# Kernel tuning notes

Measured on AMD Instinct MI355X. Metric: run time of the kernel, lower is better.

The kernel has to match this reference:

```python
import jax, jax.numpy as jnp
import numpy as np

B, N, T, NIN = 2048, 8, 20, 2
ES, HS, NL, NEMB = 64, 128, 3, 64


def setup_inputs() -> dict:
    key = jax.random.key(0)
    ks = jax.random.split(key, 12)
    def nrm(k, shape, scale=1.0):
        return jax.random.normal(k, shape, dtype=jnp.float32) * scale
    s_in = 1.0 / np.sqrt(HS)
    return {
        "x": nrm(ks[0], (B, N, T, NIN)),
        "pos_enc_agents": nrm(ks[1], (N,)),
        "pos_enc_time": nrm(ks[2], (T,)),
        "emb_W": nrm(ks[3], (ES, NIN), 1.0 / np.sqrt(NIN)),
        "emb_b": nrm(ks[4], (ES,), 0.01),
        "Wih0": nrm(ks[5], (3 * HS, ES), s_in),
        "Wih_rest": nrm(ks[6], (NL - 1, 3 * HS, HS), s_in),
        "Whh": nrm(ks[7], (NL, 3 * HS, HS), s_in),
        "bih": nrm(ks[8], (NL, 3 * HS), s_in),
        "bhh": nrm(ks[9], (NL, 3 * HS), s_in),
        "out_W": nrm(ks[10], (NEMB, HS), s_in),
        "out_b": nrm(ks[11], (NEMB,), 0.01),
    }


def _gru_layer(xs, Wih, Whh, bih, bhh):
    # xs: [M, T, in]; PyTorch GRU gate order (r, z, n)
    gi = jnp.einsum('mti,gi->mtg', xs, Wih) + bih  # precompute input gates [M,T,3H]
    H = Whh.shape[-1]

    def step(h, g):
        gh = h @ Whh.T + bhh
        ir, iz, inn = jnp.split(g, 3, axis=-1)
        hr, hz, hn = jnp.split(gh, 3, axis=-1)
        r = jax.nn.sigmoid(ir + hr)
        z = jax.nn.sigmoid(iz + hz)
        n = jnp.tanh(inn + r * hn)
        h_new = (1.0 - z) * n + z * h
        return h_new, h_new

    h0 = jnp.zeros((xs.shape[0], H), xs.dtype)
    hT, ys = jax.lax.scan(step, h0, jnp.swapaxes(gi, 0, 1))
    return jnp.swapaxes(ys, 0, 1), hT  # [M,T,H], [M,H]


def reference(x, pos_enc_agents, pos_enc_time, emb_W, emb_b,
              Wih0, Wih_rest, Whh, bih, bhh, out_W, out_b):
    b, n, t, _ = x.shape
    # positional encoding broadcast over batch and coord dims (p=2)
    pe = pos_enc_time[None, None, :, None] + pos_enc_agents[None, :, None, None]
    xe = jax.nn.relu(jnp.einsum('bntp,ep->bnte', x + pe, emb_W) + emb_b)
    # fold agents into batch: each agent starts from zero hidden state
    h = xe.reshape(b * n, t, -1)
    finals = []
    ys, hT = _gru_layer(h, Wih0, Whh[0], bih[0], bhh[0])
    finals.append(hT)
    for l in range(Wih_rest.shape[0]):
        ys, hT = _gru_layer(ys, Wih_rest[l], Whh[l + 1], bih[l + 1], bhh[l + 1])
        finals.append(hT)
    alpha = ys[:, -1]  # last timestep of top layer, [B*N, H]
    out = alpha @ out_W.T + out_b  # [B*N, nemb]
    # concat over agents along last dim, keep seq_len=1 dim like torch
    out = out.reshape(b, n * out_W.shape[0])[:, None, :]
    # hidden returned by torch is the final hidden of the LAST agent loop
    hidden = jnp.stack(finals).reshape(len(finals), b, n, -1)[:, :, -1]
    return out, hidden
```

## Files before the change

kernel.cpp:

```cpp
#include <hip/hip_runtime.h>
#include <hip/hip_bf16.h>


typedef _Float16 half8 __attribute__((ext_vector_type(8)));
typedef _Float16 half4 __attribute__((ext_vector_type(4)));
typedef float floatx4 __attribute__((ext_vector_type(4)));

#define MFMA16(a, b, c) __builtin_amdgcn_mfma_f32_16x16x32_f16((a), (b), (c), 0, 0, 0)

static __device__ __forceinline__ float ldin(const void* p, long i, bool f32) {
    return f32 ? ((const float*)p)[i]
               : __bfloat162float(((const __hip_bfloat16*)p)[i]);
}

static __device__ __forceinline__ bool detect_f32(const void* peT, const void* x) {
    const __hip_bfloat16* a = (const __hip_bfloat16*)peT;
    const __hip_bfloat16* b = (const __hip_bfloat16*)x;
    bool weird = false;
    for (int i = 0; i < 20; i++) {
        float v = fabsf(__bfloat162float(a[i]));
        if (!(v == 0.0f || (v > 1e-8f && v < 1e8f))) weird = true;
    }
    for (int i = 0; i < 64; i++) {
        float v = fabsf(__bfloat162float(b[i]));
        if (!(v == 0.0f || (v > 1e-8f && v < 1e8f))) weird = true;
    }
    return weird;
}

static __device__ __forceinline__ float fsigm(float x) {
    x = fminf(fmaxf(x, -60.f), 60.f);
    float e = __builtin_amdgcn_exp2f(-1.442695041f * x);
    return __builtin_amdgcn_rcpf(1.0f + e);
}
static __device__ __forceinline__ float ftanh(float x) {
    x = fminf(fmaxf(x, -30.f), 30.f);
    float e = __builtin_amdgcn_exp2f(2.885390082f * x);
    return 1.0f - 2.0f * __builtin_amdgcn_rcpf(1.0f + e);
}

__global__ __launch_bounds__(64) void prepack_kernel(
    const void* __restrict__ Whh,
    const void* __restrict__ WihR,
    const void* __restrict__ Wih0,
    const void* __restrict__ outW,
    const void* __restrict__ peT,
    const void* __restrict__ x,
    _Float16* __restrict__ ws)
{
    const bool f32 = detect_f32(peT, x);
    int fid  = blockIdx.x;
    int lane = threadIdx.x;
    int nlo = lane & 15, quad = lane >> 4;
    const void* src;
    long base;
    int row, k0, ldk;
    if (fid < 288) {
        int l = fid / 96, r = fid % 96;
        int ks = r & 3, q1 = r >> 2, g = q1 % 3, ctile = q1 / 3;
        row = g * 128 + ctile * 16 + nlo; k0 = ks * 32 + quad * 8; ldk = 128;
        src = Whh; base = (long)l * 384 * 128;
    } else if (fid < 480) {
        int f = fid - 288; int l = f / 96, r = f % 96;
        int ks = r & 3, q1 = r >> 2, g = q1 % 3, ctile = q1 / 3;
        row = g * 128 + ctile * 16 + nlo; k0 = ks * 32 + quad * 8; ldk = 128;
        src = WihR; base = (long)l * 384 * 128;
    } else if (fid < 528) {
        int r = fid - 480;
        int ks = r & 1, q1 = r >> 1, g = q1 % 3, ctile = q1 / 3;
        row = g * 128 + ctile * 16 + nlo; k0 = ks * 32 + quad * 8; ldk = 64;
        src = Wih0; base = 0;
    } else {
        int r = fid - 528; int ks = r & 3, ot = r >> 2;
        row = ot * 16 + nlo; k0 = ks * 32 + quad * 8; ldk = 128;
        src = outW; base = 0;
    }
    _Float16* d = ws + (long)fid * 512 + lane * 8;
#pragma unroll
    for (int j = 0; j < 8; j++)
        d[j] = (_Float16)ldin(src, base + (long)row * ldk + k0 + j, f32);
}

__global__ __launch_bounds__(768, 3) void rnn_fused(
    const void* __restrict__ x,
    const void* __restrict__ peA,
    const void* __restrict__ peT,
    const void* __restrict__ embW,
    const void* __restrict__ embB,
    const void* __restrict__ bih,
    const void* __restrict__ bhh,
    const void* __restrict__ outB,
    const _Float16* __restrict__ ws,
    float* __restrict__ out)
{
    __shared__ __align__(16) _Float16 hA[3][2][64][136];
    __shared__ __align__(16) _Float16 eA[2][64][72];
    __shared__ float emb0[64], emb1[64], embb[64];
    __shared__ float biasS[1536];

    const bool f32 = detect_f32(peT, x);

    const int tid  = threadIdx.x;
    const int w    = tid >> 6;
    const int lane = tid & 63;
    const int nlo  = lane & 15;
    const int quad = lane >> 4;
    const int qk   = quad * 8;
    const int m0   = blockIdx.x * 64;
    const int rot  = blockIdx.x & 3;
    const int ctr  = (blockIdx.x >> 2) & 1;

    for (int i = tid; i < 3 * 2 * 64 * 136; i += 768)
        (&hA[0][0][0][0])[i] = (_Float16)0.f;
    if (tid < 64) {
        emb0[tid] = ldin(embW, tid * 2 + 0, f32);
        emb1[tid] = ldin(embW, tid * 2 + 1, f32);
        embb[tid] = ldin(embB, tid, f32);
    }
    for (int idx = tid; idx < 1536; idx += 768) {
        int l = idx >> 9, r = idx & 511, g = r >> 7, c = r & 127;
        float v;
        if      (g == 0) v = ldin(bih, l * 384 + c, f32)       + ldin(bhh, l * 384 + c, f32);
        else if (g == 1) v = ldin(bih, l * 384 + 128 + c, f32) + ldin(bhh, l * 384 + 128 + c, f32);
        else if (g == 2) v = ldin(bih, l * 384 + 256 + c, f32);
        else             v = ldin(bhh, l * 384 + 256 + c, f32);
        biasS[idx] = v;
    }

    const int em = tid >> 2;
    const int ej = (tid & 3) * 16;
    const float peAg = ldin(peA, ((m0 + em) & 7), f32);

    __syncthreads();

#pragma unroll 1
    for (int s = 0; s < 23; s++) {
        const int l = w >> 2;
        const int W = w & 3;
        const int t = s - 1 - l;
        if (t >= 0 && t < 20) {
            const int p = (t + 1) & 1;
            const int q = t & 1;
            const int KGI = (l == 0) ? 2 : 4;
            const _Float16* inBase = (l == 0) ? &eA[t & 1][0][0]
                                              : &hA[l - 1][t & 1][0][0];
            const int inStride = (l == 0) ? 72 : 136;

#pragma unroll
            for (int ct0 = 0; ct0 < 2; ct0++) {
                const int c8 = W * 2 + ((ct0 + ctr) & 1);
                const int c4 = c8 * 16 + quad * 4;

                floatx4 acc[4][4];
#pragma unroll
                for (int g = 0; g < 4; g++) {
                    floatx4 b = *(const floatx4*)&biasS[(l * 4 + g) * 128 + c4];
#pragma unroll
                    for (int rt = 0; rt < 4; rt++) acc[g][rt] = b;
                }
#pragma unroll
                for (int ks0 = 0; ks0 < 4; ks0++) {
                    const int ks = (ks0 + rot) & 3;
                    half8 B0 = *(const half8*)&hA[l][p][0 * 16 + nlo][ks * 32 + qk];
                    half8 B1 = *(const half8*)&hA[l][p][1 * 16 + nlo][ks * 32 + qk];
                    half8 B2 = *(const half8*)&hA[l][p][2 * 16 + nlo][ks * 32 + qk];
                    half8 B3 = *(const half8*)&hA[l][p][3 * 16 + nlo][ks * 32 + qk];
#pragma unroll
                    for (int g = 0; g < 3; g++) {
                        const int ai = (g == 2) ? 3 : g;
                        half8 Wf = *(const half8*)(ws +
                            ((long)(l * 96 + (c8 * 3 + g) * 4 + ks)) * 512 + lane * 8);
                        acc[ai][0] = MFMA16(Wf, B0, acc[ai][0]);
                        acc[ai][1] = MFMA16(Wf, B1, acc[ai][1]);
                        acc[ai][2] = MFMA16(Wf, B2, acc[ai][2]);
                        acc[ai][3] = MFMA16(Wf, B3, acc[ai][3]);
                    }
                }
                for (int ks0 = 0; ks0 < KGI; ks0++) {
                    const int ks = (ks0 + rot) & (KGI - 1);
                    half8 B0 = *(const half8*)(inBase + (0 * 16 + nlo) * inStride + ks * 32 + qk);
                    half8 B1 = *(const half8*)(inBase + (1 * 16 + nlo) * inStride + ks * 32 + qk);
                    half8 B2 = *(const half8*)(inBase + (2 * 16 + nlo) * inStride + ks * 32 + qk);
                    half8 B3 = *(const half8*)(inBase + (3 * 16 + nlo) * inStride + ks * 32 + qk);
#pragma unroll
                    for (int g = 0; g < 3; g++) {
                        long f = (l == 0) ? (long)(480 + (c8 * 3 + g) * 2 + ks)
                                          : (long)(288 + (l - 1) * 96 + (c8 * 3 + g) * 4 + ks);
                        half8 Uf = *(const half8*)(ws + f * 512 + lane * 8);
                        acc[g][0] = MFMA16(Uf, B0, acc[g][0]);
                        acc[g][1] = MFMA16(Uf, B1, acc[g][1]);
                        acc[g][2] = MFMA16(Uf, B2, acc[g][2]);
                        acc[g][3] = MFMA16(Uf, B3, acc[g][3]);
                    }
                }
#pragma unroll
                for (int rt = 0; rt < 4; rt++) {
                    half4 ho = *(const half4*)&hA[l][p][rt * 16 + nlo][c4];
                    half4 hn;
#pragma unroll
                    for (int rg = 0; rg < 4; rg++) {
                        float r = fsigm(acc[0][rt][rg]);
                        float z = fsigm(acc[1][rt][rg]);
                        float n = ftanh(acc[2][rt][rg] + r * acc[3][rt][rg]);
                        hn[rg] = (_Float16)(n + z * ((float)ho[rg] - n));
                    }
                    *(half4*)&hA[l][q][rt * 16 + nlo][c4] = hn;
                }
            }
        }
        if (l == 0 && s < 20) {
            float x0 = ldin(x, ((long)(m0 + em) * 20 + s) * 2 + 0, f32);
            float x1 = ldin(x, ((long)(m0 + em) * 20 + s) * 2 + 1, f32);
            float pe = ldin(peT, s, f32) + peAg;
            float xp0 = x0 + pe, xp1 = x1 + pe;
#pragma unroll
            for (int jj = 0; jj < 16; jj++) {
                float e = fmaf(emb0[ej + jj], xp0, fmaf(emb1[ej + jj], xp1, embb[ej + jj]));
                eA[s & 1][em][ej + jj] = (_Float16)fmaxf(e, 0.f);
            }
        }
        __syncthreads();
    }

    if (w < 8) {
        const int otile = w & 3;
        const int rtb   = (w >> 2) * 2;
        half8 Ao[4];
#pragma unroll
        for (int ks = 0; ks < 4; ks++)
            Ao[ks] = *(const half8*)(ws + ((long)(528 + otile * 4 + ks)) * 512 + lane * 8);
        floatx4 ob;
#pragma unroll
        for (int rg = 0; rg < 4; rg++) ob[rg] = ldin(outB, otile * 16 + quad * 4 + rg, f32);
#pragma unroll
        for (int rr = 0; rr < 2; rr++) {
            const int rt = rtb + rr;
            floatx4 acc = ob;
#pragma unroll
            for (int ks = 0; ks < 4; ks++) {
                half8 b = *(const half8*)&hA[2][1][rt * 16 + nlo][ks * 32 + qk];
                acc = MFMA16(Ao[ks], b, acc);
            }
            *(floatx4*)&out[(long)(m0 + rt * 16 + nlo) * 64 + otile * 16 + quad * 4] = acc;
        }
    }

    for (int idx = tid; idx < 3 * 8 * 128; idx += 768) {
        int l2 = idx >> 10, r = idx & 1023, si = r >> 7, k = r & 127;
        int sq = si * 8 + 7;
        long m = m0 + sq;
        out[1048576L + ((long)l2 * 2048 + (m >> 3)) * 128 + k] =
            (float)hA[l2][1][sq][k];
    }
}

extern "C" void kernel_launch(void* const* d_in, const int* in_sizes, int n_in,
                              void* d_out, int out_size, void* d_ws, size_t ws_size,
                              hipStream_t stream)
{
    int ix = 0, ipeA = 1, ipeT = 2, iembW = 3, iembB = 4, iWih0 = 5, iWihR = 6,
        iWhh = 7, ibih = 8, ibhh = 9, ioutW = 10, ioutB = 11;
    int f64 = -1, s64 = -1, f1152 = -1, s1152 = -1;
    for (int i = 0; i < n_in; i++) {
        int s = in_sizes[i];
        if      (s == 655360) ix = i;
        else if (s == 8)      ipeA = i;
        else if (s == 20)     ipeT = i;
        else if (s == 128)    iembW = i;
        else if (s == 24576)  iWih0 = i;
        else if (s == 98304)  iWihR = i;
        else if (s == 147456) iWhh = i;
        else if (s == 8192)   ioutW = i;
        else if (s == 64)     { if (f64 < 0) f64 = i; else s64 = i; }
        else if (s == 1152)   { if (f1152 < 0) f1152 = i; else s1152 = i; }
    }
    if (f64 >= 0)   { iembB = f64;  ioutB = (s64  >= 0 ? s64  : f64); }
    if (f1152 >= 0) { ibih = f1152; ibhh = (s1152 >= 0 ? s1152 : f1152); }

    _Float16* ws = (_Float16*)d_ws;
    float* out = (float*)d_out;

    hipLaunchKernelGGL(prepack_kernel, dim3(544), dim3(64), 0, stream,
                       d_in[iWhh], d_in[iWihR], d_in[iWih0], d_in[ioutW],
                       d_in[ipeT], d_in[ix], ws);
    hipLaunchKernelGGL(rnn_fused, dim3(256), dim3(768), 0, stream,
                       d_in[ix], d_in[ipeA], d_in[ipeT], d_in[iembW], d_in[iembB],
                       d_in[ibih], d_in[ibhh], d_in[ioutB], ws, out);
}
```

Baseline: 380.6 us.

## Cache half of recurrent weights in registers, specialize layer paths, vectorize embedding stores

Preloads the first two K-slices of each warp's recurrent weight fragments into registers before the time loop, so each step reads only half of them from global memory. It drops the per-block rotation of K/column order and splits the input-projection loop into separate compile-time unrolled paths for layer 0 and higher layers. It also removes the input clamps in sigmoid/tanh and writes the embedding output as half8 vector stores. The extra registers may lower occupancy or cause spills, and removing the rotation may bring back LDS or cache contention that it was there to spread.

Measured after the change: 526.1 us. 38.2% more time.

```diff
diff --git a/kernel.cpp b/kernel.cpp
--- a/kernel.cpp
+++ b/kernel.cpp
@@ -29,12 +29,10 @@
 }
 
 static __device__ __forceinline__ float fsigm(float x) {
-    x = fminf(fmaxf(x, -60.f), 60.f);
     float e = __builtin_amdgcn_exp2f(-1.442695041f * x);
     return __builtin_amdgcn_rcpf(1.0f + e);
 }
 static __device__ __forceinline__ float ftanh(float x) {
-    x = fminf(fmaxf(x, -30.f), 30.f);
     float e = __builtin_amdgcn_exp2f(2.885390082f * x);
     return 1.0f - 2.0f * __builtin_amdgcn_rcpf(1.0f + e);
 }
@@ -107,8 +105,8 @@
     const int quad = lane >> 4;
     const int qk   = quad * 8;
     const int m0   = blockIdx.x * 64;
-    const int rot  = blockIdx.x & 3;
-    const int ctr  = (blockIdx.x >> 2) & 1;
+    const int l    = w >> 2;
+    const int W    = w & 3;
 
     for (int i = tid; i < 3 * 2 * 64 * 136; i += 768)
         (&hA[0][0][0][0])[i] = (_Float16)0.f;
@@ -118,14 +116,24 @@
         embb[tid] = ldin(embB, tid, f32);
     }
     for (int idx = tid; idx < 1536; idx += 768) {
-        int l = idx >> 9, r = idx & 511, g = r >> 7, c = r & 127;
+        int ll = idx >> 9, r = idx & 511, g = r >> 7, c = r & 127;
         float v;
-        if      (g == 0) v = ldin(bih, l * 384 + c, f32)       + ldin(bhh, l * 384 + c, f32);
-        else if (g == 1) v = ldin(bih, l * 384 + 128 + c, f32) + ldin(bhh, l * 384 + 128 + c, f32);
-        else if (g == 2) v = ldin(bih, l * 384 + 256 + c, f32);
-        else             v = ldin(bhh, l * 384 + 256 + c, f32);
+        if      (g == 0) v = ldin(bih, ll * 384 + c, f32)       + ldin(bhh, ll * 384 + c, f32);
+        else if (g == 1) v = ldin(bih, ll * 384 + 128 + c, f32) + ldin(bhh, ll * 384 + 128 + c, f32);
+        else if (g == 2) v = ldin(bih, ll * 384 + 256 + c, f32);
+        else             v = ldin(bhh, ll * 384 + 256 + c, f32);
         biasS[idx] = v;
     }
+
+    half8 WghC[2][3][2];
+#pragma unroll
+    for (int ct = 0; ct < 2; ct++)
+#pragma unroll
+        for (int g = 0; g < 3; g++)
+#pragma unroll
+            for (int ks = 0; ks < 2; ks++)
+                WghC[ct][g][ks] = *(const half8*)(ws +
+                    ((long)(l * 96 + ((W * 2 + ct) * 3 + g) * 4 + ks)) * 512 + lane * 8);
 
     const int em = tid >> 2;
     const int ej = (tid & 3) * 16;
@@ -135,20 +143,14 @@
 
 #pragma unroll 1
     for (int s = 0; s < 23; s++) {
-        const int l = w >> 2;
-        const int W = w & 3;
         const int t = s - 1 - l;
         if (t >= 0 && t < 20) {
             const int p = (t + 1) & 1;
             const int q = t & 1;
-            const int KGI = (l == 0) ? 2 : 4;
-            const _Float16* inBase = (l == 0) ? &eA[t & 1][0][0]
-                                              : &hA[l - 1][t & 1][0][0];
-            const int inStride = (l == 0) ? 72 : 136;
 
 #pragma unroll
             for (int ct0 = 0; ct0 < 2; ct0++) {
-                const int c8 = W * 2 + ((ct0 + ctr) & 1);
+                const int c8 = W * 2 + ct0;
                 const int c4 = c8 * 16 + quad * 4;
 
                 floatx4 acc[4][4];
@@ -159,8 +161,7 @@
                     for (int rt = 0; rt < 4; rt++) acc[g][rt] = b;
                 }
 #pragma unroll
-                for (int ks0 = 0; ks0 < 4; ks0++) {
-                    const int ks = (ks0 + rot) & 3;
+                for (int ks = 0; ks < 4; ks++) {
                     half8 B0 = *(const half8*)&hA[l][p][0 * 16 + nlo][ks * 32 + qk];
                     half8 B1 = *(const half8*)&hA[l][p][1 * 16 + nlo][ks * 32 + qk];
                     half8 B2 = *(const half8*)&hA[l][p][2 * 16 + nlo][ks * 32 + qk];
@@ -168,29 +169,52 @@
 #pragma unroll
                     for (int g = 0; g < 3; g++) {
                         const int ai = (g == 2) ? 3 : g;
-                        half8 Wf = *(const half8*)(ws +
-                            ((long)(l * 96 + (c8 * 3 + g) * 4 + ks)) * 512 + lane * 8);
+                        half8 Wf;
+                        if (ks < 2) {
+                            Wf = WghC[ct0][g][ks];
+                        } else {
+                            Wf = *(const half8*)(ws +
+                                ((long)(l * 96 + (c8 * 3 + g) * 4 + ks)) * 512 + lane * 8);
+                        }
                         acc[ai][0] = MFMA16(Wf, B0, acc[ai][0]);
                         acc[ai][1] = MFMA16(Wf, B1, acc[ai][1]);
                         acc[ai][2] = MFMA16(Wf, B2, acc[ai][2]);
                         acc[ai][3] = MFMA16(Wf, B3, acc[ai][3]);
                     }
                 }
-                for (int ks0 = 0; ks0 < KGI; ks0++) {
-                    const int ks = (ks0 + rot) & (KGI - 1);
-                    half8 B0 = *(const half8*)(inBase + (0 * 16 + nlo) * inStride + ks * 32 + qk);
-                    half8 B1 = *(const half8*)(inBase + (1 * 16 + nlo) * inStride + ks * 32 + qk);
-                    half8 B2 = *(const half8*)(inBase + (2 * 16 + nlo) * inStride + ks * 32 + qk);
-                    half8 B3 = *(const half8*)(inBase + (3 * 16 + nlo) * inStride + ks * 32 + qk);
-#pragma unroll
-                    for (int g = 0; g < 3; g++) {
-                        long f = (l == 0) ? (long)(480 + (c8 * 3 + g) * 2 + ks)
-                                          : (long)(288 + (l - 1) * 96 + (c8 * 3 + g) * 4 + ks);
-                        half8 Uf = *(const half8*)(ws + f * 512 + lane * 8);
-                        acc[g][0] = MFMA16(Uf, B0, acc[g][0]);
-                        acc[g][1] = MFMA16(Uf, B1, acc[g][1]);
-                        acc[g][2] = MFMA16(Uf, B2, acc[g][2]);
-                        acc[g][3] = MFMA16(Uf, B3, acc[g][3]);
+                if (l == 0) {
+#pragma unroll
+                    for (int ks = 0; ks < 2; ks++) {
+                        half8 B0 = *(const half8*)&eA[t & 1][0 * 16 + nlo][ks * 32 + qk];
+                        half8 B1 = *(const half8*)&eA[t & 1][1 * 16 + nlo][ks * 32 + qk];
+                        half8 B2 = *(const half8*)&eA[t & 1][2 * 16 + nlo][ks * 32 + qk];
+                        half8 B3 = *(const half8*)&eA[t & 1][3 * 16 + nlo][ks * 32 + qk];
+#pragma unroll
+                        for (int g = 0; g < 3; g++) {
+                            half8 Uf = *(const half8*)(ws +
+                                ((long)(480 + (c8 * 3 + g) * 2 + ks)) * 512 + lane * 8);
+                            acc[g][0] = MFMA16(Uf, B0, acc[g][0]);
+                            acc[g][1] = MFMA16(Uf, B1, acc[g][1]);
+                            acc[g][2] = MFMA16(Uf, B2, acc[g][2]);
+                            acc[g][3] = MFMA16(Uf, B3, acc[g][3]);
+                        }
+                    }
+                } else {
+#pragma unroll
+                    for (int ks = 0; ks < 4; ks++) {
+                        half8 B0 = *(const half8*)&hA[l - 1][t & 1][0 * 16 + nlo][ks * 32 + qk];
+                        half8 B1 = *(const half8*)&hA[l - 1][t & 1][1 * 16 + nlo][ks * 32 + qk];
+                        half8 B2 = *(const half8*)&hA[l - 1][t & 1][2 * 16 + nlo][ks * 32 + qk];
+                        half8 B3 = *(const half8*)&hA[l - 1][t & 1][3 * 16 + nlo][ks * 32 + qk];
+#pragma unroll
+                        for (int g = 0; g < 3; g++) {
+                            half8 Uf = *(const half8*)(ws +
+                                ((long)(288 + (l - 1) * 96 + (c8 * 3 + g) * 4 + ks)) * 512 + lane * 8);
+                            acc[g][0] = MFMA16(Uf, B0, acc[g][0]);
+                            acc[g][1] = MFMA16(Uf, B1, acc[g][1]);
+                            acc[g][2] = MFMA16(Uf, B2, acc[g][2]);
+                            acc[g][3] = MFMA16(Uf, B3, acc[g][3]);
+                        }
                     }
                 }
 #pragma unroll
@@ -213,11 +237,16 @@
             float x1 = ldin(x, ((long)(m0 + em) * 20 + s) * 2 + 1, f32);
             float pe = ldin(peT, s, f32) + peAg;
             float xp0 = x0 + pe, xp1 = x1 + pe;
-#pragma unroll
-            for (int jj = 0; jj < 16; jj++) {
-                float e = fmaf(emb0[ej + jj], xp0, fmaf(emb1[ej + jj], xp1, embb[ej + jj]));
-                eA[s & 1][em][ej + jj] = (_Float16)fmaxf(e, 0.f);
+            half8 v0, v1;
+#pragma unroll
+            for (int jj = 0; jj < 8; jj++) {
+                float e0 = fmaf(emb0[ej + jj], xp0, fmaf(emb1[ej + jj], xp1, embb[ej + jj]));
+                float e1 = fmaf(emb0[ej + 8 + jj], xp0, fmaf(emb1[ej + 8 + jj], xp1, embb[ej + 8 + jj]));
+                v0[jj] = (_Float16)fmaxf(e0, 0.f);
+                v1[jj] = (_Float16)fmaxf(e1, 0.f);
             }
+            *(half8*)&eA[s & 1][em][ej]     = v0;
+            *(half8*)&eA[s & 1][em][ej + 8] = v1;
         }
         __syncthreads();
     }
```
